# Performance work log

Hardware: AMD Instinct MI355X
Metric: run time of the kernel (lower is better)

## Reference

```python
import jax, jax.numpy as jnp
import numpy as np

H = 2048
V = 50257
M = 64

def setup_inputs() -> dict:
    key = jax.random.key(0)
    ks = jax.random.split(key, 14)
    s = 0.02  # weight init scale for numerical sanity
    return {
        "input_tok": jax.random.randint(ks[0], (1,), 0, V),
        "hidden": jax.random.normal(ks[1], (1, 1, H), jnp.float32),
        "encoder_outputs": jax.random.normal(ks[2], (M, H), jnp.float32),
        "emb": jax.random.normal(ks[3], (V, H), jnp.float32) * s,
        "attn_w": jax.random.normal(ks[4], (M, 2 * H), jnp.float32) * s,
        "attn_b": jax.random.normal(ks[5], (M,), jnp.float32) * s,
        "comb_w": jax.random.normal(ks[6], (H, 2 * H), jnp.float32) * s,
        "comb_b": jax.random.normal(ks[7], (H,), jnp.float32) * s,
        "w_ih": jax.random.normal(ks[8], (3 * H, H), jnp.float32) * s,
        "w_hh": jax.random.normal(ks[9], (3 * H, H), jnp.float32) * s,
        "b_ih": jax.random.normal(ks[10], (3 * H,), jnp.float32) * s,
        "b_hh": jax.random.normal(ks[11], (3 * H,), jnp.float32) * s,
        "out_w": jax.random.normal(ks[12], (V, H), jnp.float32) * s,
        "out_b": jax.random.normal(ks[13], (V,), jnp.float32) * s,
    }

def reference(input_tok, hidden, encoder_outputs, emb, attn_w, attn_b,
              comb_w, comb_b, w_ih, w_hh, b_ih, b_hh, out_w, out_b):
    # embedded: [1, H] (dropout is eval-mode identity)
    embedded = emb[input_tok].reshape(1, H)
    h0 = hidden[0]  # [1, H]
    # Bahdanau-style attention over encoder outputs
    attn_weights = jax.nn.softmax(
        jnp.concatenate([embedded, h0], axis=1) @ attn_w.T + attn_b, axis=1)  # [1, M]
    attn_applied = attn_weights @ encoder_outputs  # [1, H]
    # combine + relu
    x = jnp.concatenate([embedded, attn_applied], axis=1) @ comb_w.T + comb_b
    x = jax.nn.relu(x)  # [1, H] -> GRU input
    # single GRU cell step, PyTorch gate order (r, z, n)
    gi = x @ w_ih.T + b_ih   # [1, 3H]
    gh = h0 @ w_hh.T + b_hh  # [1, 3H]
    i_r, i_z, i_n = jnp.split(gi, 3, axis=1)
    h_r, h_z, h_n = jnp.split(gh, 3, axis=1)
    r = jax.nn.sigmoid(i_r + h_r)
    z = jax.nn.sigmoid(i_z + h_z)
    n = jnp.tanh(i_n + r * h_n)
    h_new = (1.0 - z) * n + z * h0  # [1, H]
    # output projection + log-softmax over vocab
    log_probs = jax.nn.log_softmax(h_new @ out_w.T + out_b, axis=1)  # [1, V]
    return (log_probs, h_new[None], attn_weights)
```

## Files before the change

### kernel.cpp

```cpp
#include <hip/hip_runtime.h>
#include <math.h>

#define H 2048
#define V 50257
#define M 64

#define NEG_BIG (-1.0e30f)

#define RPW 13
#define NB5 967
#define NB6 197

__device__ inline float wred_sum(float v) {
#pragma unroll
    for (int o = 32; o >= 1; o >>= 1) v += __shfl_down(v, o);
    return v;
}

__global__ void k_scores(const int* __restrict__ tok, const float* __restrict__ hidden,
                         const float* __restrict__ emb, const float* __restrict__ attn_w,
                         const float* __restrict__ attn_b, float* __restrict__ scores) {
    const int m = blockIdx.x;
    const int t = threadIdx.x;
    const float* erow = emb + (size_t)tok[0] * H;
    const float4* w4 = (const float4*)(attn_w + (size_t)m * 2 * H);
    float acc = 0.f;
    for (int i = t; i < 1024; i += 256) {
        float4 w = w4[i];
        int k = i * 4;
        float4 c = (k < H) ? *(const float4*)(erow + k)
                           : *(const float4*)(hidden + (k - H));
        acc += w.x * c.x + w.y * c.y + w.z * c.z + w.w * c.w;
    }
    __shared__ float sred[4];
    float s = wred_sum(acc);
    int wid = t >> 6, lane = t & 63;
    if (lane == 0) sred[wid] = s;
    __syncthreads();
    if (t == 0) scores[m] = sred[0] + sred[1] + sred[2] + sred[3] + attn_b[m];
}

__global__ void k_sm_aa(const float* __restrict__ scores, const float* __restrict__ enc,
                        float* __restrict__ aw_out, float* __restrict__ attn_applied) {
    __shared__ float w[M];
    int t = threadIdx.x;
    if (t < 64) {
        float s = scores[t];
        float mx = s;
#pragma unroll
        for (int o = 32; o >= 1; o >>= 1) mx = fmaxf(mx, __shfl_xor(mx, o));
        float e = expf(s - mx);
        float sum = e;
#pragma unroll
        for (int o = 32; o >= 1; o >>= 1) sum += __shfl_xor(sum, o);
        float aw = e / sum;
        w[t] = aw;
        if (blockIdx.x == 0) aw_out[t] = aw;
    }
    __syncthreads();
    int h = blockIdx.x * 256 + t;
    float acc = 0.f;
#pragma unroll 8
    for (int m = 0; m < M; ++m) acc += w[m] * enc[(size_t)m * H + h];
    attn_applied[h] = acc;
}

__global__ void k_combine(const int* __restrict__ tok, const float* __restrict__ emb,
                          const float* __restrict__ comb_w, const float* __restrict__ comb_b,
                          const float* __restrict__ aa, float* __restrict__ x_out) {
    int r = (blockIdx.x * blockDim.x + threadIdx.x) >> 6;
    int lane = threadIdx.x & 63;
    const float* erow = emb + (size_t)tok[0] * H;
    const float4* w4 = (const float4*)(comb_w + (size_t)r * 2 * H);
    float acc = 0.f;
#pragma unroll
    for (int it = 0; it < 16; ++it) {
        int i = it * 64 + lane;
        float4 w = w4[i];
        int k = i * 4;
        float4 c = (k < H) ? *(const float4*)(erow + k)
                           : *(const float4*)(aa + (k - H));
        acc += w.x * c.x + w.y * c.y + w.z * c.z + w.w * c.w;
    }
    acc = wred_sum(acc);
    if (lane == 0) x_out[r] = fmaxf(acc + comb_b[r], 0.f);
}

__global__ void k_gru(const float* __restrict__ hidden, const float* __restrict__ w_ih,
                      const float* __restrict__ w_hh, const float* __restrict__ b_ih,
                      const float* __restrict__ b_hh, const float* __restrict__ x,
                      float* __restrict__ h_out) {
    int j = (blockIdx.x * blockDim.x + threadIdx.x) >> 6;
    int lane = threadIdx.x & 63;
    const float4* x4 = (const float4*)x;
    const float4* h4 = (const float4*)hidden;
    const float4* wir = (const float4*)(w_ih + (size_t)j * H);
    const float4* wiz = (const float4*)(w_ih + (size_t)(H + j) * H);
    const float4* win = (const float4*)(w_ih + (size_t)(2 * H + j) * H);
    const float4* whr = (const float4*)(w_hh + (size_t)j * H);
    const float4* whz = (const float4*)(w_hh + (size_t)(H + j) * H);
    const float4* whn = (const float4*)(w_hh + (size_t)(2 * H + j) * H);
    float air = 0, aiz = 0, ain = 0, ahr = 0, ahz = 0, ahn = 0;
#pragma unroll
    for (int it = 0; it < 8; ++it) {
        int i = it * 64 + lane;
        float4 xv = x4[i], hv = h4[i];
        float4 a;
        a = wir[i]; air += a.x * xv.x + a.y * xv.y + a.z * xv.z + a.w * xv.w;
        a = wiz[i]; aiz += a.x * xv.x + a.y * xv.y + a.z * xv.z + a.w * xv.w;
        a = win[i]; ain += a.x * xv.x + a.y * xv.y + a.z * xv.z + a.w * xv.w;
        a = whr[i]; ahr += a.x * hv.x + a.y * hv.y + a.z * hv.z + a.w * hv.w;
        a = whz[i]; ahz += a.x * hv.x + a.y * hv.y + a.z * hv.z + a.w * hv.w;
        a = whn[i]; ahn += a.x * hv.x + a.y * hv.y + a.z * hv.z + a.w * hv.w;
    }
    air = wred_sum(air); aiz = wred_sum(aiz); ain = wred_sum(ain);
    ahr = wred_sum(ahr); ahz = wred_sum(ahz); ahn = wred_sum(ahn);
    if (lane == 0) {
        float r = 1.f / (1.f + expf(-(air + b_ih[j] + ahr + b_hh[j])));
        float z = 1.f / (1.f + expf(-(aiz + b_ih[H + j] + ahz + b_hh[H + j])));
        float n = tanhf(ain + b_ih[2 * H + j] + r * (ahn + b_hh[2 * H + j]));
        h_out[j] = (1.f - z) * n + z * hidden[j];
    }
}

__global__ void k_logits(const float* __restrict__ out_w, const float* __restrict__ out_b,
                         const float* __restrict__ hnew, float* __restrict__ logits,
                         float2* __restrict__ part) {
    const int t = threadIdx.x;
    const int lane = t & 63, wid = t >> 6;
    const int gw = blockIdx.x * 4 + wid;
    const int base = gw * RPW;

    const float4* h4 = (const float4*)hnew;
    float4 h[8];
#pragma unroll
    for (int it = 0; it < 8; ++it) h[it] = h4[it * 64 + lane];

    float m = NEG_BIG, s = 0.f;
#pragma unroll
    for (int r = 0; r < RPW; ++r) {
        int row = base + r;
        if (row >= V) break;
        const float4* w4 = (const float4*)(out_w + (size_t)row * H);
        float acc = 0.f;
#pragma unroll
        for (int it = 0; it < 8; ++it) {
            float4 w = w4[it * 64 + lane];
            acc += w.x * h[it].x + w.y * h[it].y + w.z * h[it].z + w.w * h[it].w;
        }
        acc = wred_sum(acc);
        if (lane == 0) {
            float lg = acc + out_b[row];
            logits[row] = lg;
            if (lg > m) { s = s * expf(m - lg) + 1.f; m = lg; }
            else s += expf(lg - m);
        }
    }
    __shared__ float2 lms[4];
    if (lane == 0) lms[wid] = make_float2(m, s);
    __syncthreads();
    if (t == 0) {
        float gm = NEG_BIG, gs = 0.f;
#pragma unroll
        for (int i = 0; i < 4; ++i) {
            float m2 = lms[i].x, s2 = lms[i].y;
            float mm = fmaxf(gm, m2);
            gs = gs * expf(gm - mm) + s2 * expf(m2 - mm);
            gm = mm;
        }
        part[blockIdx.x] = make_float2(gm, gs);
    }
}

__global__ void k_logsoftmax(float* __restrict__ logits, const float2* __restrict__ part) {
    const int t = threadIdx.x;
    float m = NEG_BIG, s = 0.f;
    for (int i = t; i < NB5; i += 256) {
        float2 p = part[i];
        float mm = fmaxf(m, p.x);
        s = s * expf(m - mm) + p.y * expf(p.x - mm);
        m = mm;
    }
    __shared__ float sm[256], ss[256];
    sm[t] = m; ss[t] = s;
    __syncthreads();
    for (int o = 128; o >= 1; o >>= 1) {
        if (t < o) {
            float m2 = sm[t + o], s2 = ss[t + o];
            float mm = fmaxf(sm[t], m2);
            ss[t] = ss[t] * expf(sm[t] - mm) + s2 * expf(m2 - mm);
            sm[t] = mm;
        }
        __syncthreads();
    }
    float lse = sm[0] + logf(ss[0]);
    int i = blockIdx.x * 256 + t;
    if (i < V) logits[i] -= lse;
}

extern "C" void kernel_launch(void* const* d_in, const int* in_sizes, int n_in,
                              void* d_out, int out_size, void* d_ws, size_t ws_size,
                              hipStream_t stream) {
    const int*   tok     = (const int*)d_in[0];
    const float* hidden  = (const float*)d_in[1];
    const float* enc     = (const float*)d_in[2];
    const float* emb     = (const float*)d_in[3];
    const float* attn_w  = (const float*)d_in[4];
    const float* attn_b  = (const float*)d_in[5];
    const float* comb_w  = (const float*)d_in[6];
    const float* comb_b  = (const float*)d_in[7];
    const float* w_ih    = (const float*)d_in[8];
    const float* w_hh    = (const float*)d_in[9];
    const float* b_ih    = (const float*)d_in[10];
    const float* b_hh    = (const float*)d_in[11];
    const float* out_w   = (const float*)d_in[12];
    const float* out_b   = (const float*)d_in[13];

    float* out = (float*)d_out;
    float* logp  = out;
    float* hout  = out + V;
    float* awout = out + V + H;

    float* ws   = (float*)d_ws;
    float*  AA   = ws;
    float*  X    = ws + 2048;
    float*  SC   = ws + 4096;
    float2* PART = (float2*)(ws + 4224);

    k_scores    <<<64,  256, 0, stream>>>(tok, hidden, emb, attn_w, attn_b, SC);
    k_sm_aa     <<<8,   256, 0, stream>>>(SC, enc, awout, AA);
    k_combine   <<<512, 256, 0, stream>>>(tok, emb, comb_w, comb_b, AA, X);
    k_gru       <<<512, 256, 0, stream>>>(hidden, w_ih, w_hh, b_ih, b_hh, X, hout);
    k_logits    <<<NB5, 256, 0, stream>>>(out_w, out_b, hout, logp, PART);
    k_logsoftmax<<<NB6, 256, 0, stream>>>(logp, PART);
}
```

Baseline: 122.9 us.

## Overlap hidden-state GRU matvec with attention kernels, add nontemporal loads

The w_hh·h0 gate matvec does not depend on the attention or combine results, so it moves into the otherwise small attention-score and softmax kernels as extra blocks. It is split 3072 rows and 3072 rows across those two launches, which fills the GPU during phases that used to run only 64 or 8 blocks. The GRU kernel then streams only w_ih and reads the precomputed gh. Weight reads use nontemporal loads, and the logits kernel changes from 13 rows per wave to 2 rows per wave, giving many more blocks. This also raises the number of partial softmax entries the final reduction must combine.

Result: faster. 106.6 us (-13.3%).

```diff
diff --git a/kernel.cpp b/kernel.cpp
--- a/kernel.cpp
+++ b/kernel.cpp
@@ -4,12 +4,15 @@
 #define H 2048
 #define V 50257
 #define M 64
-
 #define NEG_BIG (-1.0e30f)
 
-#define RPW 13
-#define NB5 967
+#define NB5 6283
 #define NB6 197
+
+typedef float f4 __attribute__((ext_vector_type(4)));
+
+__device__ inline f4 ntload(const f4* p) { return __builtin_nontemporal_load(p); }
+__device__ inline float dot4(f4 a, f4 b) { return a.x*b.x + a.y*b.y + a.z*b.z + a.w*b.w; }
 
 __device__ inline float wred_sum(float v) {
 #pragma unroll
@@ -17,52 +20,82 @@
     return v;
 }
 
-__global__ void k_scores(const int* __restrict__ tok, const float* __restrict__ hidden,
-                         const float* __restrict__ emb, const float* __restrict__ attn_w,
-                         const float* __restrict__ attn_b, float* __restrict__ scores) {
-    const int m = blockIdx.x;
-    const int t = threadIdx.x;
-    const float* erow = emb + (size_t)tok[0] * H;
-    const float4* w4 = (const float4*)(attn_w + (size_t)m * 2 * H);
-    float acc = 0.f;
-    for (int i = t; i < 1024; i += 256) {
-        float4 w = w4[i];
-        int k = i * 4;
-        float4 c = (k < H) ? *(const float4*)(erow + k)
-                           : *(const float4*)(hidden + (k - H));
-        acc += w.x * c.x + w.y * c.y + w.z * c.z + w.w * c.w;
-    }
-    __shared__ float sred[4];
-    float s = wred_sum(acc);
-    int wid = t >> 6, lane = t & 63;
-    if (lane == 0) sred[wid] = s;
-    __syncthreads();
-    if (t == 0) scores[m] = sred[0] + sred[1] + sred[2] + sred[3] + attn_b[m];
-}
-
-__global__ void k_sm_aa(const float* __restrict__ scores, const float* __restrict__ enc,
-                        float* __restrict__ aw_out, float* __restrict__ attn_applied) {
-    __shared__ float w[M];
-    int t = threadIdx.x;
-    if (t < 64) {
-        float s = scores[t];
-        float mx = s;
-#pragma unroll
-        for (int o = 32; o >= 1; o >>= 1) mx = fmaxf(mx, __shfl_xor(mx, o));
-        float e = expf(s - mx);
-        float sum = e;
-#pragma unroll
-        for (int o = 32; o >= 1; o >>= 1) sum += __shfl_xor(sum, o);
-        float aw = e / sum;
-        w[t] = aw;
-        if (blockIdx.x == 0) aw_out[t] = aw;
-    }
-    __syncthreads();
-    int h = blockIdx.x * 256 + t;
-    float acc = 0.f;
+__global__ void k_scores_gh1(const int* __restrict__ tok, const float* __restrict__ hidden,
+                             const float* __restrict__ emb, const float* __restrict__ attn_w,
+                             const float* __restrict__ attn_b, const float* __restrict__ w_hh,
+                             const float* __restrict__ b_hh, float* __restrict__ scores,
+                             float* __restrict__ gh) {
+    const int t = threadIdx.x, lane = t & 63, wid = t >> 6;
+    if (blockIdx.x < 64) {
+        const int m = blockIdx.x;
+        const float* erow = emb + (size_t)tok[0] * H;
+        const f4* w4 = (const f4*)(attn_w + (size_t)m * 2 * H);
+        float acc = 0.f;
+        for (int i = t; i < 1024; i += 256) {
+            f4 w = ntload(w4 + i);
+            int k = i * 4;
+            f4 c = (k < H) ? *(const f4*)(erow + k) : *(const f4*)(hidden + (k - H));
+            acc += dot4(w, c);
+        }
+        __shared__ float sred[4];
+        float s = wred_sum(acc);
+        if (lane == 0) sred[wid] = s;
+        __syncthreads();
+        if (t == 0) scores[m] = sred[0] + sred[1] + sred[2] + sred[3] + attn_b[m];
+    } else {
+        const int j = (blockIdx.x - 64) * 4 + wid;
+        const f4* w4 = (const f4*)(w_hh + (size_t)j * H);
+        const f4* h4 = (const f4*)hidden;
+        float acc = 0.f;
+#pragma unroll
+        for (int it = 0; it < 8; ++it) {
+            int i = it * 64 + lane;
+            acc += dot4(ntload(w4 + i), h4[i]);
+        }
+        acc = wred_sum(acc);
+        if (lane == 0) gh[j] = acc + b_hh[j];
+    }
+}
+
+__global__ void k_sm_aa_gh2(const float* __restrict__ scores, const float* __restrict__ enc,
+                            const float* __restrict__ hidden, const float* __restrict__ w_hh,
+                            const float* __restrict__ b_hh, float* __restrict__ aw_out,
+                            float* __restrict__ attn_applied, float* __restrict__ gh) {
+    const int t = threadIdx.x, lane = t & 63, wid = t >> 6;
+    if (blockIdx.x < 8) {
+        __shared__ float w[M];
+        if (t < 64) {
+            float s = scores[t];
+            float mx = s;
+#pragma unroll
+            for (int o = 32; o >= 1; o >>= 1) mx = fmaxf(mx, __shfl_xor(mx, o));
+            float e = expf(s - mx);
+            float sum = e;
+#pragma unroll
+            for (int o = 32; o >= 1; o >>= 1) sum += __shfl_xor(sum, o);
+            float aw = e / sum;
+            w[t] = aw;
+            if (blockIdx.x == 0) aw_out[t] = aw;
+        }
+        __syncthreads();
+        int h = blockIdx.x * 256 + t;
+        float acc = 0.f;
 #pragma unroll 8
-    for (int m = 0; m < M; ++m) acc += w[m] * enc[(size_t)m * H + h];
-    attn_applied[h] = acc;
+        for (int m = 0; m < M; ++m) acc += w[m] * enc[(size_t)m * H + h];
+        attn_applied[h] = acc;
+    } else {
+        const int j = 3072 + (blockIdx.x - 8) * 4 + wid;
+        const f4* w4 = (const f4*)(w_hh + (size_t)j * H);
+        const f4* h4 = (const f4*)hidden;
+        float acc = 0.f;
+#pragma unroll
+        for (int it = 0; it < 8; ++it) {
+            int i = it * 64 + lane;
+            acc += dot4(ntload(w4 + i), h4[i]);
+        }
+        acc = wred_sum(acc);
+        if (lane == 0) gh[j] = acc + b_hh[j];
+    }
 }
 
 __global__ void k_combine(const int* __restrict__ tok, const float* __restrict__ emb,
@@ -71,54 +104,43 @@
     int r = (blockIdx.x * blockDim.x + threadIdx.x) >> 6;
     int lane = threadIdx.x & 63;
     const float* erow = emb + (size_t)tok[0] * H;
-    const float4* w4 = (const float4*)(comb_w + (size_t)r * 2 * H);
+    const f4* w4 = (const f4*)(comb_w + (size_t)r * 2 * H);
     float acc = 0.f;
 #pragma unroll
     for (int it = 0; it < 16; ++it) {
         int i = it * 64 + lane;
-        float4 w = w4[i];
+        f4 w = ntload(w4 + i);
         int k = i * 4;
-        float4 c = (k < H) ? *(const float4*)(erow + k)
-                           : *(const float4*)(aa + (k - H));
-        acc += w.x * c.x + w.y * c.y + w.z * c.z + w.w * c.w;
+        f4 c = (k < H) ? *(const f4*)(erow + k) : *(const f4*)(aa + (k - H));
+        acc += dot4(w, c);
     }
     acc = wred_sum(acc);
     if (lane == 0) x_out[r] = fmaxf(acc + comb_b[r], 0.f);
 }
 
-__global__ void k_gru(const float* __restrict__ hidden, const float* __restrict__ w_ih,
-                      const float* __restrict__ w_hh, const float* __restrict__ b_ih,
-                      const float* __restrict__ b_hh, const float* __restrict__ x,
-                      float* __restrict__ h_out) {
+__global__ void k_gates(const float* __restrict__ hidden, const float* __restrict__ w_ih,
+                        const float* __restrict__ b_ih, const float* __restrict__ x,
+                        const float* __restrict__ gh, float* __restrict__ h_out) {
     int j = (blockIdx.x * blockDim.x + threadIdx.x) >> 6;
     int lane = threadIdx.x & 63;
-    const float4* x4 = (const float4*)x;
-    const float4* h4 = (const float4*)hidden;
-    const float4* wir = (const float4*)(w_ih + (size_t)j * H);
-    const float4* wiz = (const float4*)(w_ih + (size_t)(H + j) * H);
-    const float4* win = (const float4*)(w_ih + (size_t)(2 * H + j) * H);
-    const float4* whr = (const float4*)(w_hh + (size_t)j * H);
-    const float4* whz = (const float4*)(w_hh + (size_t)(H + j) * H);
-    const float4* whn = (const float4*)(w_hh + (size_t)(2 * H + j) * H);
-    float air = 0, aiz = 0, ain = 0, ahr = 0, ahz = 0, ahn = 0;
+    const f4* x4 = (const f4*)x;
+    const f4* wr = (const f4*)(w_ih + (size_t)j * H);
+    const f4* wz = (const f4*)(w_ih + (size_t)(H + j) * H);
+    const f4* wn = (const f4*)(w_ih + (size_t)(2 * H + j) * H);
+    float ar = 0.f, az = 0.f, an = 0.f;
 #pragma unroll
     for (int it = 0; it < 8; ++it) {
         int i = it * 64 + lane;
-        float4 xv = x4[i], hv = h4[i];
-        float4 a;
-        a = wir[i]; air += a.x * xv.x + a.y * xv.y + a.z * xv.z + a.w * xv.w;
-        a = wiz[i]; aiz += a.x * xv.x + a.y * xv.y + a.z * xv.z + a.w * xv.w;
-        a = win[i]; ain += a.x * xv.x + a.y * xv.y + a.z * xv.z + a.w * xv.w;
-        a = whr[i]; ahr += a.x * hv.x + a.y * hv.y + a.z * hv.z + a.w * hv.w;
-        a = whz[i]; ahz += a.x * hv.x + a.y * hv.y + a.z * hv.z + a.w * hv.w;
-        a = whn[i]; ahn += a.x * hv.x + a.y * hv.y + a.z * hv.z + a.w * hv.w;
-    }
-    air = wred_sum(air); aiz = wred_sum(aiz); ain = wred_sum(ain);
-    ahr = wred_sum(ahr); ahz = wred_sum(ahz); ahn = wred_sum(ahn);
+        f4 xv = x4[i];
+        ar += dot4(ntload(wr + i), xv);
+        az += dot4(ntload(wz + i), xv);
+        an += dot4(ntload(wn + i), xv);
+    }
+    ar = wred_sum(ar); az = wred_sum(az); an = wred_sum(an);
     if (lane == 0) {
-        float r = 1.f / (1.f + expf(-(air + b_ih[j] + ahr + b_hh[j])));
-        float z = 1.f / (1.f + expf(-(aiz + b_ih[H + j] + ahz + b_hh[H + j])));
-        float n = tanhf(ain + b_ih[2 * H + j] + r * (ahn + b_hh[2 * H + j]));
+        float r = 1.f / (1.f + expf(-(ar + b_ih[j] + gh[j])));
+        float z = 1.f / (1.f + expf(-(az + b_ih[H + j] + gh[H + j])));
+        float n = tanhf(an + b_ih[2 * H + j] + r * gh[2 * H + j]);
         h_out[j] = (1.f - z) * n + z * hidden[j];
     }
 }
@@ -126,35 +148,27 @@
 __global__ void k_logits(const float* __restrict__ out_w, const float* __restrict__ out_b,
                          const float* __restrict__ hnew, float* __restrict__ logits,
                          float2* __restrict__ part) {
-    const int t = threadIdx.x;
-    const int lane = t & 63, wid = t >> 6;
-    const int gw = blockIdx.x * 4 + wid;
-    const int base = gw * RPW;
-
-    const float4* h4 = (const float4*)hnew;
-    float4 h[8];
-#pragma unroll
-    for (int it = 0; it < 8; ++it) h[it] = h4[it * 64 + lane];
-
+    const int t = threadIdx.x, lane = t & 63, wid = t >> 6;
+    const int base = (blockIdx.x * 4 + wid) * 2;
+    const int row0 = base, row1 = base + 1;
+    const bool v0 = row0 < V, v1 = row1 < V;
+    const f4* w0 = (const f4*)(out_w + (size_t)(v0 ? row0 : 0) * H);
+    const f4* w1 = (const f4*)(out_w + (size_t)(v1 ? row1 : 0) * H);
+    const f4* h4 = (const f4*)hnew;
+    float a0 = 0.f, a1 = 0.f;
+#pragma unroll
+    for (int it = 0; it < 8; ++it) {
+        int i = it * 64 + lane;
+        f4 h = h4[i];
+        a0 += dot4(ntload(w0 + i), h);
+        a1 += dot4(ntload(w1 + i), h);
+    }
+    a0 = wred_sum(a0); a1 = wred_sum(a1);
     float m = NEG_BIG, s = 0.f;
-#pragma unroll
-    for (int r = 0; r < RPW; ++r) {
-        int row = base + r;
-        if (row >= V) break;
-        const float4* w4 = (const float4*)(out_w + (size_t)row * H);
-        float acc = 0.f;
-#pragma unroll
-        for (int it = 0; it < 8; ++it) {
-            float4 w = w4[it * 64 + lane];
-            acc += w.x * h[it].x + w.y * h[it].y + w.z * h[it].z + w.w * h[it].w;
-        }
-        acc = wred_sum(acc);
-        if (lane == 0) {
-            float lg = acc + out_b[row];
-            logits[row] = lg;
-            if (lg > m) { s = s * expf(m - lg) + 1.f; m = lg; }
-            else s += expf(lg - m);
-        }
+    if (lane == 0) {
+        if (v0) { float lg = a0 + out_b[row0]; logits[row0] = lg; m = lg; s = 1.f; }
+        if (v1) { float lg = a1 + out_b[row1]; logits[row1] = lg;
+                  float mm = fmaxf(m, lg); s = s * expf(m - mm) + expf(lg - mm); m = mm; }
     }
     __shared__ float2 lms[4];
     if (lane == 0) lms[wid] = make_float2(m, s);
@@ -162,8 +176,8 @@
     if (t == 0) {
         float gm = NEG_BIG, gs = 0.f;
 #pragma unroll
-        for (int i = 0; i < 4; ++i) {
-            float m2 = lms[i].x, s2 = lms[i].y;
+        for (int i2 = 0; i2 < 4; ++i2) {
+            float m2 = lms[i2].x, s2 = lms[i2].y;
             float mm = fmaxf(gm, m2);
             gs = gs * expf(gm - mm) + s2 * expf(m2 - mm);
             gm = mm;
@@ -221,16 +235,17 @@
     float* hout  = out + V;
     float* awout = out + V + H;
 
-    float* ws   = (float*)d_ws;
+    float* ws = (float*)d_ws;
     float*  AA   = ws;
     float*  X    = ws + 2048;
     float*  SC   = ws + 4096;
-    float2* PART = (float2*)(ws + 4224);
-
-    k_scores    <<<64,  256, 0, stream>>>(tok, hidden, emb, attn_w, attn_b, SC);
-    k_sm_aa     <<<8,   256, 0, stream>>>(SC, enc, awout, AA);
+    float*  GH   = ws + 4160;
+    float2* PART = (float2*)(ws + 10304);
+
+    k_scores_gh1<<<832, 256, 0, stream>>>(tok, hidden, emb, attn_w, attn_b, w_hh, b_hh, SC, GH);
+    k_sm_aa_gh2 <<<776, 256, 0, stream>>>(SC, enc, hidden, w_hh, b_hh, awout, AA, GH);
     k_combine   <<<512, 256, 0, stream>>>(tok, emb, comb_w, comb_b, AA, X);
-    k_gru       <<<512, 256, 0, stream>>>(hidden, w_ih, w_hh, b_ih, b_hh, X, hout);
+    k_gates     <<<512, 256, 0, stream>>>(hidden, w_ih, b_ih, X, GH, hout);
     k_logits    <<<NB5, 256, 0, stream>>>(out_w, out_b, hout, logp, PART);
     k_logsoftmax<<<NB6, 256, 0, stream>>>(logp, PART);
 }
```
